# Optimization experiments

Hardware: AMD Instinct MI355X
Metric: run time of the kernel (lower is better)

## Reference

```python
import jax, jax.numpy as jnp
import numpy as np
from functools import partial


@partial(jax.custom_vjp, nondiff_argnums=(1,))
def binarize1d(x, upper):
    return jnp.round(jnp.clip(x, 0.0, upper))

def _b1_fwd(x, upper):
    return jnp.round(jnp.clip(x, 0.0, upper)), x

def _b1_bwd(upper, x, g):
    # torch Binarize.backward for 1-D input: zero grad outside [0, upper]
    return (jnp.where((x < 0.0) | (x > upper), 0.0, g),)

binarize1d.defvjp(_b1_fwd, _b1_bwd)


def binarize2d(x, upper):
    # torch Binarize.backward for >=2-D input passes grad through unchanged -> STE
    return x + jax.lax.stop_gradient(jnp.round(jnp.clip(x, 0.0, upper)) - x)


def _perm_matrices(wc, wr, C, R):
    b = binarize1d(wc, float(C - 1))  # [C] selected row index per column
    # identity_column[i,j] = i  ->  col[i,j] = 1 iff i == b[j]
    col = binarize2d(1.0 - jnp.abs(jnp.arange(C, dtype=wc.dtype)[:, None] - b[None, :]), 1.0)
    r = binarize1d(wr, float(R - 1))  # [R] selected column index per row
    # identity_row[i,j] = j  ->  row[i,j] = 1 iff j == r[i]
    row = binarize2d(1.0 - jnp.abs(jnp.arange(R, dtype=wr.dtype)[None, :] - r[:, None]), 1.0)
    return col, row, b, r


def _fix_duplicates(sel, n):
    # sel: int32 [n]. Reassign every non-first occurrence of a value to an unused
    # slot. Deterministic stand-in for the original list + random.shuffle + pop():
    # unused slots are consumed in descending order (ascending list, pop from end).
    i = jnp.arange(n)
    eq = (sel[None, :] == sel[:, None]) & (i[:, None] < i[None, :])
    dup = eq.any(axis=0)  # dup[j]: sel[j] already seen at some earlier index
    counts = jnp.zeros((n,), jnp.int32).at[sel].add(1)
    empty_desc = jnp.sort(jnp.where(counts == 0, i, -1))[::-1]
    rank = jnp.cumsum(dup.astype(jnp.int32)) - 1
    return jnp.where(dup, empty_desc[rank], sel), dup


def _forward(x, weight_column, weight_row):
    C = weight_column.shape[0]
    R = weight_row.shape[0]
    # __update_rearrange_matrix__ : build selection indices from current weights
    _, _, b, r = _perm_matrices(weight_column, weight_row, C, R)
    bi = jax.lax.stop_gradient(b).astype(jnp.int32)
    ri = jax.lax.stop_gradient(r).astype(jnp.int32)
    # __constraint_rearrange_matrix__ : in-place .data rewrite of colliding entries
    new_b, dup_c = _fix_duplicates(bi, C)
    new_r, dup_r = _fix_duplicates(ri, R)
    wc = weight_column + jax.lax.stop_gradient(
        jnp.where(dup_c, new_b.astype(weight_column.dtype), weight_column) - weight_column)
    wr = weight_row + jax.lax.stop_gradient(
        jnp.where(dup_r, new_r.astype(weight_row.dtype), weight_row) - weight_row)
    # final __update_rearrange_matrix__ with the constrained weights
    col_mat, row_mat, _, _ = _perm_matrices(wc, wr, C, R)
    out = jnp.matmul(x, col_mat)    # [B, R, C] : column permutation
    out = jnp.matmul(row_mat, out)  # [B, R, C] : row permutation
    return out


def setup_inputs():
    key = jax.random.key(0)
    k1, k2, k3 = jax.random.split(key, 3)
    B, R, C = 16, 1024, 2048
    x = jax.random.normal(k1, (B, R, C), dtype=jnp.float32)
    weight_column = jax.random.uniform(k2, (C,), dtype=jnp.float32) * C  # uniform(0, C) as in reset_parameters
    weight_row = jax.random.uniform(k3, (R,), dtype=jnp.float32) * R
    return {"x": x, "weight_column": weight_column, "weight_row": weight_row}


def reference(x, weight_column, weight_row):
    return _forward(x, weight_column, weight_row)
```

## Files before the change

### kernel.cpp

```cpp
#include <hip/hip_runtime.h>

#define MAXN 2048

__global__ void build_map_kernel(const float* __restrict__ wc, const float* __restrict__ wr,
                                 int C, int R,
                                 int* __restrict__ colmap, int* __restrict__ rowmap) {
    const float* w;
    int n;
    int* outmap;
    if (blockIdx.x == 0) { w = wc; n = C; outmap = colmap; }
    else                 { w = wr; n = R; outmap = rowmap; }

    __shared__ int sel[MAXN];
    __shared__ int first[MAXN];
    __shared__ int emptyslot[MAXN];
    __shared__ int dts[256], ets[256];

    const int t = threadIdx.x;
    const int base = t * 8;
    const float upper = (float)(n - 1);

    for (int k = 0; k < 8; k++) {
        int idx = base + k;
        if (idx < n) {
            float v = w[idx];
            v = fminf(fmaxf(v, 0.0f), upper);
            sel[idx]   = (int)rintf(v);
            first[idx] = 0x7fffffff;
        }
    }
    __syncthreads();
    for (int k = 0; k < 8; k++) {
        int idx = base + k;
        if (idx < n) atomicMin(&first[sel[idx]], idx);
    }
    __syncthreads();

    int dflag[8], eflag[8];
    int dsum = 0, esum = 0;
    for (int k = 0; k < 8; k++) {
        int idx = base + k;
        if (idx < n) {
            dflag[k] = (first[sel[idx]] != idx) ? 1 : 0;
            eflag[k] = (first[idx] == 0x7fffffff) ? 1 : 0;
        } else { dflag[k] = 0; eflag[k] = 0; }
        dsum += dflag[k]; esum += eflag[k];
    }

    dts[t] = dsum; ets[t] = esum;
    __syncthreads();
    for (int off = 1; off < 256; off <<= 1) {
        int dv = 0, ev = 0;
        if (t >= off) { dv = dts[t - off]; ev = ets[t - off]; }
        __syncthreads();
        dts[t] += dv; ets[t] += ev;
        __syncthreads();
    }
    const int dexc = dts[t] - dsum;
    const int eexc = ets[t] - esum;
    const int E    = ets[255];

    int erun = eexc;
    for (int k = 0; k < 8; k++) {
        int idx = base + k;
        if (idx < n && eflag[k]) emptyslot[E - 1 - erun] = idx;
        erun += eflag[k];
    }
    __syncthreads();

    int drun = dexc;
    for (int k = 0; k < 8; k++) {
        int idx = base + k;
        if (idx < n) outmap[idx] = dflag[k] ? emptyslot[drun] : sel[idx];
        drun += dflag[k];
    }
}

__global__ void gather_kernel(const float* __restrict__ x,
                              const int* __restrict__ rowmap,
                              const int* __restrict__ colmap,
                              float* __restrict__ out,
                              int R, int C) {
    __shared__ float lds[MAXN];
    const int blk = blockIdx.x;
    const int b = blk / R;
    const int i = blk - b * R;
    const int sr = rowmap[i];

    const float4* src4 = (const float4*)(x + ((size_t)b * R + sr) * (size_t)C);
    float4*       dst4 = (float4*)(out + ((size_t)b * R + i) * (size_t)C);
    const int4*  cmap4 = (const int4*)colmap;

    const int t = threadIdx.x;
    const int n4 = C >> 2;

    for (int k = t; k < n4; k += 256) {
        ((float4*)lds)[k] = src4[k];
    }
    __syncthreads();
    for (int k = t; k < n4; k += 256) {
        int4 c = cmap4[k];
        float4 v;
        v.x = lds[c.x]; v.y = lds[c.y]; v.z = lds[c.z]; v.w = lds[c.w];
        dst4[k] = v;
    }
}

extern "C" void kernel_launch(void* const* d_in, const int* in_sizes, int n_in,
                              void* d_out, int out_size, void* d_ws, size_t ws_size,
                              hipStream_t stream) {
    const float* x  = (const float*)d_in[0];
    const float* wc = (const float*)d_in[1];
    const float* wr = (const float*)d_in[2];
    const int C = in_sizes[1];
    const int R = in_sizes[2];
    const int B = in_sizes[0] / (R * C);

    int* colmap = (int*)d_ws;
    int* rowmap = colmap + C;

    build_map_kernel<<<2, 256, 0, stream>>>(wc, wr, C, R, colmap, rowmap);
    gather_kernel<<<B * R, 256, 0, stream>>>(x, rowmap, colmap, (float*)d_out, R, C);
}
```

Baseline: 240.0 us.

## Process one row per wavefront with register-staged loads and no block barrier

The gather kernel now gives each 64-lane wavefront its own output row, with four rows per 256-thread block. Each wave stages its source row in its own LDS slice, so the block-wide __syncthreads is removed. All eight float4 loads per lane are issued into registers before any LDS store, which puts more memory requests in flight. The cost is 32KB of LDS per block, which may limit how many blocks fit on a CU, and it relies on a wave writing and reading its own LDS slice without a barrier.

```diff
diff --git a/kernel.cpp b/kernel.cpp
--- a/kernel.cpp
+++ b/kernel.cpp
@@ -76,33 +76,49 @@
     }
 }
 
-__global__ void gather_kernel(const float* __restrict__ x,
-                              const int* __restrict__ rowmap,
-                              const int* __restrict__ colmap,
-                              float* __restrict__ out,
-                              int R, int C) {
-    __shared__ float lds[MAXN];
-    const int blk = blockIdx.x;
-    const int b = blk / R;
-    const int i = blk - b * R;
+__global__ __launch_bounds__(256) void gather_kernel(
+        const float* __restrict__ x,
+        const int* __restrict__ rowmap,
+        const int* __restrict__ colmap,
+        float* __restrict__ out,
+        int R, int C, int total) {
+    __shared__ float lds[4 * MAXN];
+    const int wave = threadIdx.x >> 6;
+    const int lane = threadIdx.x & 63;
+    const int row = blockIdx.x * 4 + wave;
+    if (row >= total) return;
+
+    const int b = row / R;
+    const int i = row - b * R;
     const int sr = rowmap[i];
 
-    const float4* src4 = (const float4*)(x + ((size_t)b * R + sr) * (size_t)C);
-    float4*       dst4 = (float4*)(out + ((size_t)b * R + i) * (size_t)C);
-    const int4*  cmap4 = (const int4*)colmap;
+    const float4* __restrict__ src4 = (const float4*)(x + ((size_t)b * R + sr) * (size_t)C);
+    float4*       __restrict__ dst4 = (float4*)(out + (size_t)row * (size_t)C);
+    const int4*   __restrict__ cmap4 = (const int4*)colmap;
 
-    const int t = threadIdx.x;
+    float* wlds = lds + wave * MAXN;
     const int n4 = C >> 2;
 
-    for (int k = t; k < n4; k += 256) {
-        ((float4*)lds)[k] = src4[k];
+    float4 v[8];
+    #pragma unroll
+    for (int k = 0; k < 8; k++) {
+        int idx = lane + 64 * k;
+        if (idx < n4) v[k] = src4[idx];
     }
-    __syncthreads();
-    for (int k = t; k < n4; k += 256) {
-        int4 c = cmap4[k];
-        float4 v;
-        v.x = lds[c.x]; v.y = lds[c.y]; v.z = lds[c.z]; v.w = lds[c.w];
-        dst4[k] = v;
+    #pragma unroll
+    for (int k = 0; k < 8; k++) {
+        int idx = lane + 64 * k;
+        if (idx < n4) ((float4*)wlds)[idx] = v[k];
+    }
+    #pragma unroll
+    for (int k = 0; k < 8; k++) {
+        int idx = lane + 64 * k;
+        if (idx < n4) {
+            int4 c = cmap4[idx];
+            float4 o;
+            o.x = wlds[c.x]; o.y = wlds[c.y]; o.z = wlds[c.z]; o.w = wlds[c.w];
+            dst4[idx] = o;
+        }
     }
 }
 
@@ -119,6 +135,8 @@
     int* colmap = (int*)d_ws;
     int* rowmap = colmap + C;
 
+    const int total = B * R;
     build_map_kernel<<<2, 256, 0, stream>>>(wc, wr, C, R, colmap, rowmap);
-    gather_kernel<<<B * R, 256, 0, stream>>>(x, rowmap, colmap, (float*)d_out, R, C);
+    gather_kernel<<<(total + 3) / 4, 256, 0, stream>>>(x, rowmap, colmap,
+                                                       (float*)d_out, R, C, total);
 }
```

New measurement: 275.9 us. 15.0% more time.
